# Optimization experiments

Measured on AMD Instinct MI355X. Metric: run time of the kernel, lower is better.

Reference implementation:

```python
import jax, jax.numpy as jnp
import numpy as np

S, B, D, H, WIN, L = 8192, 4, 512, 8, 64, 6
HD = D // H
EPS = 1e-5


def setup_inputs() -> dict:
    key = jax.random.key(0)
    ks = jax.random.split(key, 6)
    s = 0.02
    return {
        "src": jax.random.normal(ks[0], (S, B, D), jnp.float32),
        "Wqkv": jax.random.normal(ks[1], (L, 3 * D, D), jnp.float32) * s,
        "bqkv": jnp.zeros((L, 3 * D), jnp.float32),
        "Wo": jax.random.normal(ks[2], (L, D, D), jnp.float32) * s,
        "bo": jnp.zeros((L, D), jnp.float32),
        "W1": jax.random.normal(ks[3], (L, 4 * D, D), jnp.float32) * s,
        "bf1": jnp.zeros((L, 4 * D), jnp.float32),
        "W2": jax.random.normal(ks[4], (L, D, 4 * D), jnp.float32) * s,
        "bf2": jnp.zeros((L, D), jnp.float32),
        "g1": jnp.ones((L, D), jnp.float32),
        "beta1": jnp.zeros((L, D), jnp.float32),
        "g2": jnp.ones((L, D), jnp.float32),
        "beta2": jnp.zeros((L, D), jnp.float32),
    }


def layernorm(x, g, b):
    m = jnp.mean(x, axis=-1, keepdims=True)
    v = jnp.mean(jnp.square(x - m), axis=-1, keepdims=True)
    return (x - m) * jax.lax.rsqrt(v + EPS) * g + b


def _forward(src, Wqkv, bqkv, Wo, bo, W1, bf1, W2, bf2, g1, beta1, g2, beta2):
    NW = S // WIN
    scale = 1.0 / np.sqrt(HD)
    x = src
    for l in range(L):
        qkv = x @ Wqkv[l].T + bqkv[l]                      # (S,B,3D)
        q, k, v = jnp.split(qkv, 3, axis=-1)
        win = lambda t: t.reshape(NW, WIN, B, H, HD)       # (NW,W,B,H,hd)
        q = win(q) * scale
        k = win(k)
        v = win(v)
        att = jax.nn.softmax(jnp.einsum('nqbhd,nkbhd->nbhqk', q, k), axis=-1)
        o = jnp.einsum('nbhqk,nkbhd->nqbhd', att, v).reshape(S, B, D)
        o = o @ Wo[l].T + bo[l]
        x = layernorm(x + o, g1[l], beta1[l])
        # FFN with ReLU (hidden = 4*d_model)
        f = jax.nn.relu(x @ W1[l].T + bf1[l]) @ W2[l].T + bf2[l]
        x = layernorm(x + f, g2[l], beta2[l])
    return x


def reference(src, Wqkv, bqkv, Wo, bo, W1, bf1, W2, bf2, g1, beta1, g2, beta2):
    return _forward(src, Wqkv, bqkv, Wo, bo, W1, bf1, W2, bf2, g1, beta1, g2, beta2)
```

## Files before the change

### kernel.cpp

```cpp
#include <hip/hip_runtime.h>
#include <hip/hip_bf16.h>

typedef __bf16 bf16x8 __attribute__((ext_vector_type(8)));
typedef float f32x4 __attribute__((ext_vector_type(4)));

static constexpr int NT = 32768;
static constexpr int D_ = 512;
static constexpr int D3 = 1536;
static constexpr int DF = 2048;
static constexpr int L_ = 6;

#define AS1 __attribute__((address_space(1)))
#define AS3 __attribute__((address_space(3)))

__device__ __forceinline__ void gload_lds16(const void* g, void* l) {
  __builtin_amdgcn_global_load_lds((const AS1 void*)g, (AS3 void*)l, 16, 0, 0);
}

template<int K, int NTN, bool RELU>
__global__ __launch_bounds__(512, 2) void gemm256(
    const __hip_bfloat16* __restrict__ A,
    const __hip_bfloat16* __restrict__ W,
    const float* __restrict__ bias,
    __hip_bfloat16* __restrict__ Cout) {
  __shared__ __align__(16) char lds[131072];
  const int t = threadIdx.x;
  const int l = t & 63, w = t >> 6;
  const int lrow = l & 15, lhi = l >> 4;
  const int wr = w >> 2, wc = w & 3;

  const int lin = blockIdx.x;
  const int wg = (lin & 7) * ((int)gridDim.x >> 3) + (lin >> 3);
  const int tm0 = (wg / NTN) * 256, tn0 = (wg % NTN) * 256;

  constexpr int NKT = K / 64;
  constexpr int NIT = NKT / 2;
  constexpr int N = NTN * 256;

  const int srow = t >> 3;
  const int sun = t & 7;

  const int u8 = (sun ^ (srow & 7)) << 3;
  const __hip_bfloat16* sA = A + (size_t)(tm0 + srow) * K + u8;
  const __hip_bfloat16* sA2 = sA + (size_t)128 * K;
  const __hip_bfloat16* sW = W + (size_t)(tn0 + srow) * K + u8;
  const __hip_bfloat16* sW2 = sW + (size_t)128 * K;

  const int lo = lrow * 128;
  const int x0 = (lhi ^ (lrow & 7)) << 4;
  const int x1 = ((4 + lhi) ^ (lrow & 7)) << 4;
  const char* pA[2][2];
  const char* pB[2][2];
  pA[0][0] = lds + (0 * 4 + wr) * 16384 + lo + x0;
  pA[0][1] = lds + (0 * 4 + wr) * 16384 + lo + x1;
  pA[1][0] = lds + (1 * 4 + wr) * 16384 + lo + x0;
  pA[1][1] = lds + (1 * 4 + wr) * 16384 + lo + x1;
  const int bo = (wc & 1) * 8192 + lo;
  pB[0][0] = lds + (0 * 4 + 2 + (wc >> 1)) * 16384 + bo + x0;
  pB[0][1] = lds + (0 * 4 + 2 + (wc >> 1)) * 16384 + bo + x1;
  pB[1][0] = lds + (1 * 4 + 2 + (wc >> 1)) * 16384 + bo + x0;
  pB[1][1] = lds + (1 * 4 + 2 + (wc >> 1)) * 16384 + bo + x1;

  auto stage = [&](int buf, int reg, const __hip_bfloat16* s, int kt) {
    char* dst = lds + (buf * 4 + reg) * 16384 + w * 1024;
    const __hip_bfloat16* src = s + kt * 64;
    gload_lds16(src, dst);
    gload_lds16(src + (size_t)64 * K, dst + 8192);
  };

  f32x4 acc[8][4] = {};
  bf16x8 bfrag[4][2], afrag[2][2];

  stage(0, 2, sW, 0);
  stage(0, 3, sW2, 0);
  stage(0, 0, sA, 0);
  stage(0, 1, sA2, 0);
  stage(1, 2, sW, 1);
  stage(1, 3, sW2, 1);
  asm volatile("s_waitcnt vmcnt(4)" ::: "memory");
  __builtin_amdgcn_s_barrier();

#define GPHASE(BUF, MB, RB, STG, VMS)                                       \
  {                                                                          \
    if (RB) {                                                                \
      _Pragma("unroll") for (int n = 0; n < 4; ++n)                          \
          _Pragma("unroll") for (int ks = 0; ks < 2; ++ks)                   \
              bfrag[n][ks] = *(const bf16x8*)(pB[BUF][ks] + n * 2048);       \
    }                                                                        \
    _Pragma("unroll") for (int ks = 0; ks < 2; ++ks) {                       \
      afrag[0][ks] = *(const bf16x8*)(pA[BUF][ks] + MB * 2048);              \
      afrag[1][ks] = *(const bf16x8*)(pA[BUF][ks] + (MB + 1) * 2048);        \
    }                                                                        \
    STG;                                                                     \
    VMS;                                                                     \
    __builtin_amdgcn_sched_barrier(0);                                       \
    __builtin_amdgcn_s_barrier();                                            \
    asm volatile("s_waitcnt lgkmcnt(0)" ::: "memory");                       \
    __builtin_amdgcn_sched_barrier(0);                                       \
    __builtin_amdgcn_s_setprio(1);                                           \
    _Pragma("unroll") for (int n = 0; n < 4; ++n)                            \
        _Pragma("unroll") for (int ks = 0; ks < 2; ++ks) {                   \
      acc[MB][n] = __builtin_amdgcn_mfma_f32_16x16x32_bf16(                  \
          afrag[0][ks], bfrag[n][ks], acc[MB][n], 0, 0, 0);                  \
      acc[MB + 1][n] = __builtin_amdgcn_mfma_f32_16x16x32_bf16(              \
          afrag[1][ks], bfrag[n][ks], acc[MB + 1][n], 0, 0, 0);              \
    }                                                                        \
    __builtin_amdgcn_s_setprio(0);                                           \
    __builtin_amdgcn_sched_barrier(0);                                       \
    __builtin_amdgcn_s_barrier();                                            \
  }

#define VM_CNT                                              \
  if (more) {                                               \
    asm volatile("s_waitcnt vmcnt(4)" ::: "memory");        \
  } else {                                                  \
    asm volatile("s_waitcnt vmcnt(0)" ::: "memory");        \
  }

  for (int it = 0; it < NIT; ++it) {
    const int t1 = 2 * it + 1;
    const bool more = (it + 1 < NIT);
    GPHASE(0, 0, 1, { stage(1, 0, sA, t1); stage(1, 1, sA2, t1); }, );
    GPHASE(0, 2, 0, { if (more) stage(0, 2, sW, t1 + 1); }, );
    GPHASE(0, 4, 0, { if (more) stage(0, 3, sW2, t1 + 1); }, );
    GPHASE(0, 6, 0, , VM_CNT);
    GPHASE(1, 0, 1, { if (more) stage(0, 0, sA, t1 + 1); }, );
    GPHASE(1, 2, 0, { if (more) stage(0, 1, sA2, t1 + 1); }, );
    GPHASE(1, 4, 0, { if (more) stage(1, 2, sW, t1 + 2); }, );
    GPHASE(1, 6, 0, { if (more) stage(1, 3, sW2, t1 + 2); }, VM_CNT);
  }
#undef GPHASE
#undef VM_CNT

  char* ep = lds + w * 16384;
#pragma unroll
  for (int n = 0; n < 4; ++n) {
    float bv = bias[tn0 + wc * 64 + n * 16 + lrow];
#pragma unroll
    for (int m = 0; m < 8; ++m)
#pragma unroll
      for (int j = 0; j < 4; ++j) {
        float v = acc[m][n][j] + bv;
        if (RELU) v = fmaxf(v, 0.f);
        int row = m * 16 + lhi * 4 + j;
        int col = n * 16 + lrow;
        *(__hip_bfloat16*)(ep + row * 128 + (((col >> 3) ^ (row & 7)) << 4) +
                           (col & 7) * 2) = __float2bfloat16(v);
      }
  }
  __builtin_amdgcn_sched_barrier(0);
  const int er = l >> 3, ec = l & 7;
#pragma unroll
  for (int p = 0; p < 16; ++p) {
    int r = p * 8 + er;
    uint4 vv = *(const uint4*)(ep + r * 128 + ((ec ^ (r & 7)) << 4));
    *(uint4*)&Cout[(size_t)(tm0 + wr * 128 + r) * N + tn0 + wc * 64 + ec * 8] = vv;
  }
}

__global__ __launch_bounds__(128) void attn_win(
    const __hip_bfloat16* __restrict__ qkv, __hip_bfloat16* __restrict__ o) {
  __shared__ __align__(16) char lds[2 * 18432];
  const int t = threadIdx.x, l = t & 63, w = t >> 6;
  char* vt = lds + w * 18432;
  char* pl = vt + 9216;
  const int wid = blockIdx.x * 2 + w;
  const int h = wid & 7, b = (wid >> 3) & 3, nw = wid >> 5;
  const int lrow = l & 15, lhi = l >> 4;
  const __hip_bfloat16* qp = qkv + (size_t)(nw * 256 + b) * 1536 + h * 64;
  const __hip_bfloat16* kp = qp + 512;
  const __hip_bfloat16* vp = qp + 1024;

  {
    const int d0 = (l & 7) * 8;
    const int r0 = l >> 3;
#pragma unroll
    for (int i = 0; i < 8; ++i) {
      int r = r0 + i * 8;
      union { uint4 u; __hip_bfloat16 e[8]; } vv;
      vv.u = *(const uint4*)(vp + (size_t)r * 6144 + d0);
#pragma unroll
      for (int j = 0; j < 8; ++j)
        *(__hip_bfloat16*)(vt + ((d0 + j) * 72 + r) * 2) = vv.e[j];
    }
  }

  bf16x8 qf[4][2], kf[4][2];
#pragma unroll
  for (int mi = 0; mi < 4; ++mi)
#pragma unroll
    for (int ks = 0; ks < 2; ++ks) {
      int r = mi * 16 + lrow;
      int d = ks * 32 + lhi * 8;
      qf[mi][ks] = __builtin_bit_cast(bf16x8, *(const uint4*)(qp + (size_t)r * 6144 + d));
      kf[mi][ks] = __builtin_bit_cast(bf16x8, *(const uint4*)(kp + (size_t)r * 6144 + d));
    }

  f32x4 s[4][4] = {};
#pragma unroll
  for (int mi = 0; mi < 4; ++mi)
#pragma unroll
    for (int ni = 0; ni < 4; ++ni) {
      s[mi][ni] = __builtin_amdgcn_mfma_f32_16x16x32_bf16(qf[mi][0], kf[ni][0], s[mi][ni], 0, 0, 0);
      s[mi][ni] = __builtin_amdgcn_mfma_f32_16x16x32_bf16(qf[mi][1], kf[ni][1], s[mi][ni], 0, 0, 0);
    }

#pragma unroll
  for (int mi = 0; mi < 4; ++mi)
#pragma unroll
    for (int j = 0; j < 4; ++j) {
      float mx = s[mi][0][j];
#pragma unroll
      for (int ni = 1; ni < 4; ++ni) mx = fmaxf(mx, s[mi][ni][j]);
      mx = fmaxf(mx, __shfl_xor(mx, 1));
      mx = fmaxf(mx, __shfl_xor(mx, 2));
      mx = fmaxf(mx, __shfl_xor(mx, 4));
      mx = fmaxf(mx, __shfl_xor(mx, 8));
      float p[4], sum = 0.f;
#pragma unroll
      for (int ni = 0; ni < 4; ++ni) { p[ni] = __expf(s[mi][ni][j] - mx); sum += p[ni]; }
      sum += __shfl_xor(sum, 1);
      sum += __shfl_xor(sum, 2);
      sum += __shfl_xor(sum, 4);
      sum += __shfl_xor(sum, 8);
      float inv = 1.f / sum;
      int row = mi * 16 + lhi * 4 + j;
#pragma unroll
      for (int ni = 0; ni < 4; ++ni)
        *(__hip_bfloat16*)(pl + (row * 72 + ni * 16 + lrow) * 2) =
            __float2bfloat16(p[ni] * inv);
    }

  bf16x8 pf[4][2], vf[4][2];
#pragma unroll
  for (int mi = 0; mi < 4; ++mi)
#pragma unroll
    for (int ks = 0; ks < 2; ++ks)
      pf[mi][ks] = *(const bf16x8*)(pl + ((mi * 16 + lrow) * 72 + ks * 32 + lhi * 8) * 2);
#pragma unroll
  for (int ni = 0; ni < 4; ++ni)
#pragma unroll
    for (int ks = 0; ks < 2; ++ks)
      vf[ni][ks] = *(const bf16x8*)(vt + ((ni * 16 + lrow) * 72 + ks * 32 + lhi * 8) * 2);

  f32x4 acc[4][4] = {};
#pragma unroll
  for (int mi = 0; mi < 4; ++mi)
#pragma unroll
    for (int ni = 0; ni < 4; ++ni) {
      acc[mi][ni] = __builtin_amdgcn_mfma_f32_16x16x32_bf16(pf[mi][0], vf[ni][0], acc[mi][ni], 0, 0, 0);
      acc[mi][ni] = __builtin_amdgcn_mfma_f32_16x16x32_bf16(pf[mi][1], vf[ni][1], acc[mi][ni], 0, 0, 0);
    }

  __hip_bfloat16* op = o + (size_t)(nw * 256 + b) * 512 + h * 64;
#pragma unroll
  for (int mi = 0; mi < 4; ++mi)
#pragma unroll
    for (int ni = 0; ni < 4; ++ni) {
      int col = ni * 16 + lrow;
#pragma unroll
      for (int j = 0; j < 4; ++j) {
        int row = mi * 16 + lhi * 4 + j;
        op[(size_t)row * 2048 + col] = __float2bfloat16(acc[mi][ni][j]);
      }
    }
}

__global__ __launch_bounds__(256) void ln_res(
    float* __restrict__ x, const __hip_bfloat16* __restrict__ f,
    const float* __restrict__ g, const float* __restrict__ be,
    __hip_bfloat16* __restrict__ xb) {
  const int w = threadIdx.x >> 6, l = threadIdx.x & 63;
  const size_t row = (size_t)blockIdx.x * 4 + w;
  float* xr = x + row * 512;
  const int c = l * 8;
  float4 a0 = *(const float4*)(xr + c);
  float4 a1 = *(const float4*)(xr + c + 4);
  union { uint4 u; __hip_bfloat16 e[8]; } fb;
  fb.u = *(const uint4*)(f + row * 512 + c);
  float v[8] = {a0.x + __bfloat162float(fb.e[0]), a0.y + __bfloat162float(fb.e[1]),
                a0.z + __bfloat162float(fb.e[2]), a0.w + __bfloat162float(fb.e[3]),
                a1.x + __bfloat162float(fb.e[4]), a1.y + __bfloat162float(fb.e[5]),
                a1.z + __bfloat162float(fb.e[6]), a1.w + __bfloat162float(fb.e[7])};
  float sum = 0.f, sq = 0.f;
#pragma unroll
  for (int j = 0; j < 8; ++j) { sum += v[j]; sq += v[j] * v[j]; }
#pragma unroll
  for (int m = 1; m < 64; m <<= 1) {
    sum += __shfl_xor(sum, m);
    sq += __shfl_xor(sq, m);
  }
  float mean = sum * (1.f / 512.f);
  float var = sq * (1.f / 512.f) - mean * mean;
  float rs = rsqrtf(var + 1e-5f);
  float4 g0 = *(const float4*)(g + c);
  float4 g1v = *(const float4*)(g + c + 4);
  float4 e0 = *(const float4*)(be + c);
  float4 e1 = *(const float4*)(be + c + 4);
  float gg[8] = {g0.x, g0.y, g0.z, g0.w, g1v.x, g1v.y, g1v.z, g1v.w};
  float ee[8] = {e0.x, e0.y, e0.z, e0.w, e1.x, e1.y, e1.z, e1.w};
  float y[8];
  __hip_bfloat16 hb[8];
#pragma unroll
  for (int j = 0; j < 8; ++j) {
    y[j] = (v[j] - mean) * rs * gg[j] + ee[j];
    hb[j] = __float2bfloat16(y[j]);
  }
  float4 o0 = {y[0], y[1], y[2], y[3]};
  float4 o1 = {y[4], y[5], y[6], y[7]};
  *(float4*)(xr + c) = o0;
  *(float4*)(xr + c + 4) = o1;
  *(uint4*)((char*)(xb + row * 512 + c)) = *(uint4*)hb;
}

__global__ void bfc(const float* __restrict__ xm, __hip_bfloat16* __restrict__ xb) {
  int i = blockIdx.x * 256 + threadIdx.x;
  float4 v = ((const float4*)xm)[i];
  __hip_bfloat16 hb[4] = {__float2bfloat16(v.x), __float2bfloat16(v.y),
                          __float2bfloat16(v.z), __float2bfloat16(v.w)};
  ((uint2*)xb)[i] = *(uint2*)hb;
}

__global__ void convq(const float* __restrict__ wq, __hip_bfloat16* __restrict__ o) {
  int i = blockIdx.x * 256 + threadIdx.x;
  float4 v = ((const float4*)wq)[i];
  int e = i * 4;
  float sc = (((e >> 9) % 1536) < 512) ? 0.125f : 1.f;
  __hip_bfloat16 hb[4] = {__float2bfloat16(v.x * sc), __float2bfloat16(v.y * sc),
                          __float2bfloat16(v.z * sc), __float2bfloat16(v.w * sc)};
  ((uint2*)o)[i] = *(uint2*)hb;
}

__global__ void convw(const float* __restrict__ s, __hip_bfloat16* __restrict__ o) {
  int i = blockIdx.x * 256 + threadIdx.x;
  float4 v = ((const float4*)s)[i];
  __hip_bfloat16 hb[4] = {__float2bfloat16(v.x), __float2bfloat16(v.y),
                          __float2bfloat16(v.z), __float2bfloat16(v.w)};
  ((uint2*)o)[i] = *(uint2*)hb;
}

__global__ void scaleb(const float* __restrict__ b, float* __restrict__ o) {
  int i = blockIdx.x * 256 + threadIdx.x;
  o[i] = b[i] * (((i % 1536) < 512) ? 0.125f : 1.f);
}

extern "C" void kernel_launch(void* const* d_in, const int* in_sizes, int n_in,
                              void* d_out, int out_size, void* d_ws, size_t ws_size,
                              hipStream_t stream) {
  const float* src  = (const float*)d_in[0];
  const float* Wqkv = (const float*)d_in[1];
  const float* bqkv = (const float*)d_in[2];
  const float* Wo   = (const float*)d_in[3];
  const float* bo   = (const float*)d_in[4];
  const float* W1   = (const float*)d_in[5];
  const float* bf1  = (const float*)d_in[6];
  const float* W2   = (const float*)d_in[7];
  const float* bf2  = (const float*)d_in[8];
  const float* g1   = (const float*)d_in[9];
  const float* be1  = (const float*)d_in[10];
  const float* g2   = (const float*)d_in[11];
  const float* be2  = (const float*)d_in[12];
  float* x = (float*)d_out;

  char* ws = (char*)d_ws;
  size_t off = 0;
  auto alloc = [&](size_t bytes) {
    char* p = ws + off;
    off += (bytes + 255) & ~(size_t)255;
    return p;
  };

  const size_t wq_b = (size_t)L_ * D3 * D_ * 2;
  const size_t wo_b = (size_t)L_ * D_ * D_ * 2;
  const size_t w1_b = (size_t)L_ * DF * D_ * 2;
  const size_t w2_b = (size_t)L_ * D_ * DF * 2;
  auto al = [](size_t v) { return (v + 255) & ~(size_t)255; };
  const size_t persist = al(wq_b) + al(wo_b) + al(w1_b) + al(w2_b) + al(L_ * D3 * 4);

  int CT = NT;
  while (CT > 2048 && persist + (size_t)CT * 6144 + 65536 > ws_size) CT >>= 1;

  __hip_bfloat16* wqkvb = (__hip_bfloat16*)alloc(wq_b);
  __hip_bfloat16* wob   = (__hip_bfloat16*)alloc(wo_b);
  __hip_bfloat16* w1b   = (__hip_bfloat16*)alloc(w1_b);
  __hip_bfloat16* w2b   = (__hip_bfloat16*)alloc(w2_b);
  float*          bqs   = (float*)alloc((size_t)L_ * D3 * 4);
  __hip_bfloat16* xbf   = (__hip_bfloat16*)alloc((size_t)CT * 512 * 2);
  __hip_bfloat16* R     = (__hip_bfloat16*)alloc((size_t)CT * 2048 * 2);
  __hip_bfloat16* OB    = (__hip_bfloat16*)alloc((size_t)CT * 512 * 2);

  hipMemcpyAsync(x, src, (size_t)NT * 512 * 4, hipMemcpyDeviceToDevice, stream);
  convq<<<L_ * D3 * D_ / 4 / 256, 256, 0, stream>>>(Wqkv, wqkvb);
  convw<<<L_ * D_ * D_ / 4 / 256, 256, 0, stream>>>(Wo, wob);
  convw<<<L_ * DF * D_ / 4 / 256, 256, 0, stream>>>(W1, w1b);
  convw<<<L_ * D_ * DF / 4 / 256, 256, 0, stream>>>(W2, w2b);
  scaleb<<<L_ * D3 / 256, 256, 0, stream>>>(bqkv, bqs);

  const int nch = NT / CT;
  for (int c = 0; c < nch; ++c) {
    float* xm = x + (size_t)c * CT * 512;
    bfc<<<CT / 2, 256, 0, stream>>>(xm, xbf);
    for (int l = 0; l < L_; ++l) {
      gemm256<512, 6, false><<<(CT / 256) * 6, 512, 0, stream>>>(
          xbf, wqkvb + (size_t)l * D3 * D_, bqs + l * D3, R);
      attn_win<<<CT / 16, 128, 0, stream>>>(R, OB);
      gemm256<512, 2, false><<<(CT / 256) * 2, 512, 0, stream>>>(
          OB, wob + (size_t)l * D_ * D_, bo + l * D_, R);
      ln_res<<<CT / 4, 256, 0, stream>>>(xm, R, g1 + l * D_, be1 + l * D_, xbf);
      gemm256<512, 8, true><<<(CT / 256) * 8, 512, 0, stream>>>(
          xbf, w1b + (size_t)l * DF * D_, bf1 + l * DF, R);
      gemm256<2048, 2, false><<<(CT / 256) * 2, 512, 0, stream>>>(
          R, w2b + (size_t)l * D_ * DF, bf2 + l * D_, OB);
      ln_res<<<CT / 4, 256, 0, stream>>>(xm, OB, g2 + l * D_, be2 + l * D_, xbf);
    }
  }
}
```

Before: 2.012 ms.

## Keep residual stream in bf16 and restructure GEMM main loop into four-row phases

The residual stream is now held only in bf16. Layernorm kernels read and write the bf16 copy and emit fp32 output only on the last layer, which removes the fp32 read/write traffic and the separate bf16 conversion pass. The GEMM main loop now has four phases per iteration instead of eight, each doing four M-blocks of MFMAs with one barrier. Stage issues and the vmcnt wait are reordered, which cuts barrier overhead but uses more registers for A fragments. Accumulating the residual in bf16 loses precision across layers, which risks tolerance failures.

```diff
diff --git a/kernel.cpp b/kernel.cpp
--- a/kernel.cpp
+++ b/kernel.cpp
@@ -69,7 +69,7 @@
   };
 
   f32x4 acc[8][4] = {};
-  bf16x8 bfrag[4][2], afrag[2][2];
+  bf16x8 bfrag[4][2], afrag[4][2];
 
   stage(0, 2, sW, 0);
   stage(0, 3, sW2, 0);
@@ -78,36 +78,43 @@
   stage(1, 2, sW, 1);
   stage(1, 3, sW2, 1);
   asm volatile("s_waitcnt vmcnt(4)" ::: "memory");
+  __builtin_amdgcn_sched_barrier(0);
   __builtin_amdgcn_s_barrier();
-
-#define GPHASE(BUF, MB, RB, STG, VMS)                                       \
+  __builtin_amdgcn_sched_barrier(0);
+
+#define MPHASE(BUF, RB, MB0, MB1, MB2, MB3, STG, VMS)                       \
   {                                                                          \
+    STG;                                                                     \
     if (RB) {                                                                \
       _Pragma("unroll") for (int n = 0; n < 4; ++n)                          \
           _Pragma("unroll") for (int ks = 0; ks < 2; ++ks)                   \
               bfrag[n][ks] = *(const bf16x8*)(pB[BUF][ks] + n * 2048);       \
     }                                                                        \
     _Pragma("unroll") for (int ks = 0; ks < 2; ++ks) {                       \
-      afrag[0][ks] = *(const bf16x8*)(pA[BUF][ks] + MB * 2048);              \
-      afrag[1][ks] = *(const bf16x8*)(pA[BUF][ks] + (MB + 1) * 2048);        \
+      afrag[0][ks] = *(const bf16x8*)(pA[BUF][ks] + MB0 * 2048);             \
+      afrag[1][ks] = *(const bf16x8*)(pA[BUF][ks] + MB1 * 2048);             \
+      afrag[2][ks] = *(const bf16x8*)(pA[BUF][ks] + MB2 * 2048);             \
+      afrag[3][ks] = *(const bf16x8*)(pA[BUF][ks] + MB3 * 2048);             \
     }                                                                        \
-    STG;                                                                     \
-    VMS;                                                                     \
-    __builtin_amdgcn_sched_barrier(0);                                       \
-    __builtin_amdgcn_s_barrier();                                            \
     asm volatile("s_waitcnt lgkmcnt(0)" ::: "memory");                       \
     __builtin_amdgcn_sched_barrier(0);                                       \
     __builtin_amdgcn_s_setprio(1);                                           \
     _Pragma("unroll") for (int n = 0; n < 4; ++n)                            \
         _Pragma("unroll") for (int ks = 0; ks < 2; ++ks) {                   \
-      acc[MB][n] = __builtin_amdgcn_mfma_f32_16x16x32_bf16(                  \
-          afrag[0][ks], bfrag[n][ks], acc[MB][n], 0, 0, 0);                  \
-      acc[MB + 1][n] = __builtin_amdgcn_mfma_f32_16x16x32_bf16(              \
-          afrag[1][ks], bfrag[n][ks], acc[MB + 1][n], 0, 0, 0);              \
+      acc[MB0][n] = __builtin_amdgcn_mfma_f32_16x16x32_bf16(                 \
+          afrag[0][ks], bfrag[n][ks], acc[MB0][n], 0, 0, 0);                 \
+      acc[MB1][n] = __builtin_amdgcn_mfma_f32_16x16x32_bf16(                 \
+          afrag[1][ks], bfrag[n][ks], acc[MB1][n], 0, 0, 0);                 \
+      acc[MB2][n] = __builtin_amdgcn_mfma_f32_16x16x32_bf16(                 \
+          afrag[2][ks], bfrag[n][ks], acc[MB2][n], 0, 0, 0);                 \
+      acc[MB3][n] = __builtin_amdgcn_mfma_f32_16x16x32_bf16(                 \
+          afrag[3][ks], bfrag[n][ks], acc[MB3][n], 0, 0, 0);                 \
     }                                                                        \
     __builtin_amdgcn_s_setprio(0);                                           \
+    VMS;                                                                     \
     __builtin_amdgcn_sched_barrier(0);                                       \
     __builtin_amdgcn_s_barrier();                                            \
+    __builtin_amdgcn_sched_barrier(0);                                       \
   }
 
 #define VM_CNT                                              \
@@ -120,16 +127,18 @@
   for (int it = 0; it < NIT; ++it) {
     const int t1 = 2 * it + 1;
     const bool more = (it + 1 < NIT);
-    GPHASE(0, 0, 1, { stage(1, 0, sA, t1); stage(1, 1, sA2, t1); }, );
-    GPHASE(0, 2, 0, { if (more) stage(0, 2, sW, t1 + 1); }, );
-    GPHASE(0, 4, 0, { if (more) stage(0, 3, sW2, t1 + 1); }, );
-    GPHASE(0, 6, 0, , VM_CNT);
-    GPHASE(1, 0, 1, { if (more) stage(0, 0, sA, t1 + 1); }, );
-    GPHASE(1, 2, 0, { if (more) stage(0, 1, sA2, t1 + 1); }, );
-    GPHASE(1, 4, 0, { if (more) stage(1, 2, sW, t1 + 2); }, );
-    GPHASE(1, 6, 0, { if (more) stage(1, 3, sW2, t1 + 2); }, VM_CNT);
-  }
-#undef GPHASE
+    MPHASE(0, 1, 0, 1, 2, 3,
+           { stage(1, 0, sA, t1); stage(1, 1, sA2, t1); }, );
+    MPHASE(0, 0, 4, 5, 6, 7,
+           { if (more) { stage(0, 2, sW, t1 + 1); stage(0, 3, sW2, t1 + 1); } },
+           VM_CNT);
+    MPHASE(1, 1, 0, 1, 2, 3,
+           { if (more) { stage(0, 0, sA, t1 + 1); stage(0, 1, sA2, t1 + 1); } }, );
+    MPHASE(1, 0, 4, 5, 6, 7,
+           { if (more) { stage(1, 2, sW, t1 + 2); stage(1, 3, sW2, t1 + 2); } },
+           VM_CNT);
+  }
+#undef MPHASE
 #undef VM_CNT
 
   char* ep = lds + w * 16384;
@@ -266,22 +275,21 @@
     }
 }
 
-__global__ __launch_bounds__(256) void ln_res(
-    float* __restrict__ x, const __hip_bfloat16* __restrict__ f,
+template<bool LAST>
+__global__ __launch_bounds__(256) void ln_res_b(
+    __hip_bfloat16* __restrict__ xb, const __hip_bfloat16* __restrict__ f,
     const float* __restrict__ g, const float* __restrict__ be,
-    __hip_bfloat16* __restrict__ xb) {
+    float* __restrict__ xout) {
   const int w = threadIdx.x >> 6, l = threadIdx.x & 63;
   const size_t row = (size_t)blockIdx.x * 4 + w;
-  float* xr = x + row * 512;
   const int c = l * 8;
-  float4 a0 = *(const float4*)(xr + c);
-  float4 a1 = *(const float4*)(xr + c + 4);
-  union { uint4 u; __hip_bfloat16 e[8]; } fb;
-  fb.u = *(const uint4*)(f + row * 512 + c);
-  float v[8] = {a0.x + __bfloat162float(fb.e[0]), a0.y + __bfloat162float(fb.e[1]),
-                a0.z + __bfloat162float(fb.e[2]), a0.w + __bfloat162float(fb.e[3]),
-                a1.x + __bfloat162float(fb.e[4]), a1.y + __bfloat162float(fb.e[5]),
-                a1.z + __bfloat162float(fb.e[6]), a1.w + __bfloat162float(fb.e[7])};
+  union { uint4 u; __hip_bfloat16 e[8]; } xa, fa;
+  xa.u = *(const uint4*)(xb + row * 512 + c);
+  fa.u = *(const uint4*)(f + row * 512 + c);
+  float v[8];
+#pragma unroll
+  for (int j = 0; j < 8; ++j)
+    v[j] = __bfloat162float(xa.e[j]) + __bfloat162float(fa.e[j]);
   float sum = 0.f, sq = 0.f;
 #pragma unroll
   for (int j = 0; j < 8; ++j) { sum += v[j]; sq += v[j] * v[j]; }
@@ -300,25 +308,19 @@
   float gg[8] = {g0.x, g0.y, g0.z, g0.w, g1v.x, g1v.y, g1v.z, g1v.w};
   float ee[8] = {e0.x, e0.y, e0.z, e0.w, e1.x, e1.y, e1.z, e1.w};
   float y[8];
-  __hip_bfloat16 hb[8];
+  union { uint4 u; __hip_bfloat16 e[8]; } hb;
 #pragma unroll
   for (int j = 0; j < 8; ++j) {
     y[j] = (v[j] - mean) * rs * gg[j] + ee[j];
-    hb[j] = __float2bfloat16(y[j]);
-  }
-  float4 o0 = {y[0], y[1], y[2], y[3]};
-  float4 o1 = {y[4], y[5], y[6], y[7]};
-  *(float4*)(xr + c) = o0;
-  *(float4*)(xr + c + 4) = o1;
-  *(uint4*)((char*)(xb + row * 512 + c)) = *(uint4*)hb;
-}
-
-__global__ void bfc(const float* __restrict__ xm, __hip_bfloat16* __restrict__ xb) {
-  int i = blockIdx.x * 256 + threadIdx.x;
-  float4 v = ((const float4*)xm)[i];
-  __hip_bfloat16 hb[4] = {__float2bfloat16(v.x), __float2bfloat16(v.y),
-                          __float2bfloat16(v.z), __float2bfloat16(v.w)};
-  ((uint2*)xb)[i] = *(uint2*)hb;
+    hb.e[j] = __float2bfloat16(y[j]);
+  }
+  *(uint4*)(xb + row * 512 + c) = hb.u;
+  if (LAST) {
+    float4 o0 = {y[0], y[1], y[2], y[3]};
+    float4 o1 = {y[4], y[5], y[6], y[7]};
+    *(float4*)(xout + row * 512 + c) = o0;
+    *(float4*)(xout + row * 512 + c + 4) = o1;
+  }
 }
 
 __global__ void convq(const float* __restrict__ wq, __hip_bfloat16* __restrict__ o) {
@@ -360,7 +362,7 @@
   const float* be1  = (const float*)d_in[10];
   const float* g2   = (const float*)d_in[11];
   const float* be2  = (const float*)d_in[12];
-  float* x = (float*)d_out;
+  float* xout = (float*)d_out;
 
   char* ws = (char*)d_ws;
   size_t off = 0;
@@ -374,22 +376,24 @@
   const size_t wo_b = (size_t)L_ * D_ * D_ * 2;
   const size_t w1_b = (size_t)L_ * DF * D_ * 2;
   const size_t w2_b = (size_t)L_ * D_ * DF * 2;
+  const size_t xb_b = (size_t)NT * 512 * 2;
   auto al = [](size_t v) { return (v + 255) & ~(size_t)255; };
-  const size_t persist = al(wq_b) + al(wo_b) + al(w1_b) + al(w2_b) + al(L_ * D3 * 4);
+  const size_t persist =
+      al(wq_b) + al(wo_b) + al(w1_b) + al(w2_b) + al(L_ * D3 * 4) + al(xb_b);
 
   int CT = NT;
-  while (CT > 2048 && persist + (size_t)CT * 6144 + 65536 > ws_size) CT >>= 1;
+  while (CT > 2048 && persist + (size_t)CT * 5120 + 65536 > ws_size) CT >>= 1;
 
   __hip_bfloat16* wqkvb = (__hip_bfloat16*)alloc(wq_b);
   __hip_bfloat16* wob   = (__hip_bfloat16*)alloc(wo_b);
   __hip_bfloat16* w1b   = (__hip_bfloat16*)alloc(w1_b);
   __hip_bfloat16* w2b   = (__hip_bfloat16*)alloc(w2_b);
   float*          bqs   = (float*)alloc((size_t)L_ * D3 * 4);
-  __hip_bfloat16* xbf   = (__hip_bfloat16*)alloc((size_t)CT * 512 * 2);
+  __hip_bfloat16* xb    = (__hip_bfloat16*)alloc(xb_b);
   __hip_bfloat16* R     = (__hip_bfloat16*)alloc((size_t)CT * 2048 * 2);
   __hip_bfloat16* OB    = (__hip_bfloat16*)alloc((size_t)CT * 512 * 2);
 
-  hipMemcpyAsync(x, src, (size_t)NT * 512 * 4, hipMemcpyDeviceToDevice, stream);
+  convw<<<NT * 512 / 4 / 256, 256, 0, stream>>>(src, xb);
   convq<<<L_ * D3 * D_ / 4 / 256, 256, 0, stream>>>(Wqkv, wqkvb);
   convw<<<L_ * D_ * D_ / 4 / 256, 256, 0, stream>>>(Wo, wob);
   convw<<<L_ * DF * D_ / 4 / 256, 256, 0, stream>>>(W1, w1b);
@@ -398,20 +402,26 @@
 
   const int nch = NT / CT;
   for (int c = 0; c < nch; ++c) {
-    float* xm = x + (size_t)c * CT * 512;
-    bfc<<<CT / 2, 256, 0, stream>>>(xm, xbf);
+    __hip_bfloat16* xm = xb + (size_t)c * CT * 512;
+    float* xo = xout + (size_t)c * CT * 512;
     for (int l = 0; l < L_; ++l) {
       gemm256<512, 6, false><<<(CT / 256) * 6, 512, 0, stream>>>(
-          xbf, wqkvb + (size_t)l * D3 * D_, bqs + l * D3, R);
+          xm, wqkvb + (size_t)l * D3 * D_, bqs + l * D3, R);
       attn_win<<<CT / 16, 128, 0, stream>>>(R, OB);
       gemm256<512, 2, false><<<(CT / 256) * 2, 512, 0, stream>>>(
           OB, wob + (size_t)l * D_ * D_, bo + l * D_, R);
-      ln_res<<<CT / 4, 256, 0, stream>>>(xm, R, g1 + l * D_, be1 + l * D_, xbf);
+      ln_res_b<false><<<CT / 4, 256, 0, stream>>>(xm, R, g1 + l * D_,
+                                                  be1 + l * D_, xo);
       gemm256<512, 8, true><<<(CT / 256) * 8, 512, 0, stream>>>(
-          xbf, w1b + (size_t)l * DF * D_, bf1 + l * DF, R);
+          xm, w1b + (size_t)l * DF * D_, bf1 + l * DF, R);
       gemm256<2048, 2, false><<<(CT / 256) * 2, 512, 0, stream>>>(
           R, w2b + (size_t)l * D_ * DF, bf2 + l * D_, OB);
-      ln_res<<<CT / 4, 256, 0, stream>>>(xm, OB, g2 + l * D_, be2 + l * D_, xbf);
-    }
-  }
-}
+      if (l == L_ - 1)
+        ln_res_b<true><<<CT / 4, 256, 0, stream>>>(xm, OB, g2 + l * D_,
+                                                   be2 + l * D_, xo);
+      else
+        ln_res_b<false><<<CT / 4, 256, 0, stream>>>(xm, OB, g2 + l * D_,
+                                                    be2 + l * D_, xo);
+    }
+  }
+}
```

After: 1.819 ms. 9.6% less time.
